# Optimization experiments

Hardware: AMD Instinct MI355X
Metric: run time of the kernel (lower is better)

## Reference

```python
import jax, jax.numpy as jnp
import numpy as np

N, M, D = 2048, 50000, 128


def setup_inputs() -> dict:
    key = jax.random.key(0)
    kz, kr = jax.random.split(key)
    z = jax.random.normal(kz, (N, D), dtype=jnp.float32)
    ref = jax.random.normal(kr, (M, D), dtype=jnp.float32)  # stands in for the concatenated in_dl batches
    return {"z": z, "ref": ref, "k": 10}


def reference(z, ref, k):
    # L2-normalize rows (matches z / z.norm(dim=1, keepdim=True))
    zn = z / jnp.linalg.norm(z, axis=1, keepdims=True)      # [N, D]
    rn = ref / jnp.linalg.norm(ref, axis=1, keepdims=True)  # [M, D]
    # Pairwise L2 distances via ||a||^2 + ||b||^2 - 2 a.b (same math as the
    # broadcast (rep_batch - rep_z).norm(dim=2), without the O(N*M*D) blowup).
    sq = (jnp.sum(zn * zn, axis=1)[:, None]
          + jnp.sum(rn * rn, axis=1)[None, :]
          - 2.0 * jnp.einsum('nd,md->nm', zn, rn))          # [N, M]
    dist = jnp.sqrt(jnp.maximum(sq, 1e-12))
    # Full sort along the reference axis, take the k-th smallest distance.
    return jnp.sort(dist, axis=1)[:, k]                      # [N]
```

## Files before the change

### kernel.cpp

```cpp
#include <hip/hip_runtime.h>


#define D_DIM 128
#define TQB 256
#define BR 64
#define NCH 64
#define NSUB (NCH * 32)
#define KK 11
#define NCAND 32
#define SLOTS 25
#define DNF 2816

typedef __bf16 bf16_t;
typedef bf16_t bf16x8 __attribute__((ext_vector_type(8)));
typedef float f32x16 __attribute__((ext_vector_type(16)));

__device__ __forceinline__ unsigned short f2bf(float f) {
    unsigned u = __float_as_uint(f);
    return (unsigned short)((u + 0x7fffu + ((u >> 16) & 1u)) >> 16);
}

__global__ __launch_bounds__(256) void normalize_bf16(
    const float* __restrict__ z, const float* __restrict__ ref,
    unsigned short* __restrict__ zb, unsigned short* __restrict__ rb,
    int N, int M)
{
    const int w = threadIdx.x >> 6;
    const int l = threadIdx.x & 63;
    const int row = blockIdx.x * 4 + w;
    if (row >= N + M) return;
    const float* in; unsigned short* out; int r;
    if (row < N) { in = z;   out = zb; r = row; }
    else         { in = ref; out = rb; r = row - N; }
    const float2 v = ((const float2*)in)[(size_t)r * 64 + l];
    float ss = v.x * v.x + v.y * v.y;
    #pragma unroll
    for (int off = 32; off > 0; off >>= 1) ss += __shfl_xor(ss, off);
    const float inv = rsqrtf(ss);
    ushort2 o; o.x = f2bf(v.x * inv); o.y = f2bf(v.y * inv);
    ((ushort2*)out)[(size_t)r * 64 + l] = o;
}

__device__ __forceinline__ void gld_lds16(const unsigned short* g,
                                          unsigned short* l) {
    __builtin_amdgcn_global_load_lds(
        (__attribute__((address_space(1))) void*)g,
        (__attribute__((address_space(3))) void*)l, 16, 0, 0);
}

__global__ __launch_bounds__(512) void knn_maxes(
    const unsigned short* __restrict__ zb, const unsigned short* __restrict__ rb,
    float* __restrict__ maxes, int N, int M, int chunk)
{
    __shared__ __align__(16) unsigned short Bt[2 * BR * D_DIM];

    const int nwg = 8 * NCH;
    const int bid = (int)blockIdx.x + 8 * (int)blockIdx.y;
    const int swz = (bid & 7) * (nwg >> 3) + (bid >> 3);
    const int bx = swz & 7;
    const int by = swz >> 3;

    const int t = threadIdx.x;
    const int lane = t & 63;
    const int w = t >> 6;
    const int quad = lane >> 4;
    const int ln = lane & 15;
    const int l31 = lane & 31;
    const int hi = lane >> 5;
    const int row = bx * TQB + w * 32 + l31;
    const int c0 = by * chunk;
    const int c1 = min(c0 + chunk, M);
    const int clen = c1 - c0;
    const int nt = (clen + BR - 1) / BR;

    bf16x8 qfr[8];
    #pragma unroll
    for (int ks = 0; ks < 8; ++ks)
        qfr[ks] = *(const bf16x8*)&zb[(size_t)row * D_DIM + ks * 16 + hi * 8];

    float mx[16];
    #pragma unroll
    for (int r = 0; r < 16; ++r) mx[r] = -3.0f;

    auto stage = [&](int half, int tile) {
        const int s0 = c0 + tile * BR;
        #pragma unroll
        for (int i = 0; i < 2; ++i) {
            const int r = w * 8 + i * 4 + quad;
            int g = s0 + r; if (g > M - 1) g = M - 1;
            const int sl = ln ^ (r & 15);
            gld_lds16(&rb[(size_t)g * D_DIM + sl * 8],
                      &Bt[half * (BR * D_DIM) + (w * 8 + i * 4) * D_DIM]);
        }
    };

    stage(0, 0);
    stage(1, nt > 1 ? 1 : 0);

    for (int it = 0; it < nt; ++it) {
        if (it + 1 < nt) asm volatile("s_waitcnt vmcnt(2)" ::: "memory");
        else             asm volatile("s_waitcnt vmcnt(0)" ::: "memory");
        __builtin_amdgcn_s_barrier();
        asm volatile("" ::: "memory");
        __builtin_amdgcn_sched_barrier(0);

        const int cur = it & 1;
        const unsigned short* Bc = &Bt[cur * (BR * D_DIM)];

        f32x16 acc0 = {0,0,0,0,0,0,0,0,0,0,0,0,0,0,0,0};
        f32x16 acc1 = {0,0,0,0,0,0,0,0,0,0,0,0,0,0,0,0};

        __builtin_amdgcn_s_setprio(1);
        #pragma unroll
        for (int ks = 0; ks < 8; ++ks) {
            const int sl = ((ks * 2 + hi) ^ ln) * 8;
            bf16x8 a0 = *(const bf16x8*)&Bc[(l31)      * D_DIM + sl];
            bf16x8 a1 = *(const bf16x8*)&Bc[(32 + l31) * D_DIM + sl];
            acc0 = __builtin_amdgcn_mfma_f32_32x32x16_bf16(a0, qfr[ks], acc0, 0, 0, 0);
            acc1 = __builtin_amdgcn_mfma_f32_32x32x16_bf16(a1, qfr[ks], acc1, 0, 0, 0);
        }
        __builtin_amdgcn_s_setprio(0);

        const int rem = clen - it * BR;
        if (rem >= BR) {
            #pragma unroll
            for (int r = 0; r < 16; ++r)
                mx[r] = fmaxf(mx[r], fmaxf(acc0[r], acc1[r]));
        } else {
            #pragma unroll
            for (int r = 0; r < 16; ++r) {
                const int crow = (r & 3) + 8 * (r >> 2) + 4 * hi;
                if (crow < rem)      mx[r] = fmaxf(mx[r], acc0[r]);
                if (32 + crow < rem) mx[r] = fmaxf(mx[r], acc1[r]);
            }
        }

        __builtin_amdgcn_sched_barrier(0);
        asm volatile("" ::: "memory");
        __builtin_amdgcn_s_barrier();
        if (it + 2 < nt) stage(cur, it + 2);
    }

    float* mp = &maxes[(size_t)row * NSUB + by * 32 + hi * 16];
    #pragma unroll
    for (int r4 = 0; r4 < 4; ++r4) {
        float4 v4 = { mx[r4 * 4], mx[r4 * 4 + 1], mx[r4 * 4 + 2], mx[r4 * 4 + 3] };
        *(float4*)&mp[r4 * 4] = v4;
    }
}

__device__ __forceinline__ float kth_largest_64(float* s, int kk, int lane) {
    float cur = -3.0f;
    for (int it = 0; it <= kk; ++it) {
        float m = s[0];
        #pragma unroll
        for (int off = 32; off > 0; off >>= 1) m = fmaxf(m, __shfl_xor(m, off));
        cur = m;
        unsigned long long b = __ballot(s[0] == m);
        bool owner = ((int)(__ffsll(b) - 1) == lane);
        #pragma unroll
        for (int j = 0; j < KK - 1; ++j) s[j] = owner ? s[j + 1] : s[j];
        if (owner) s[KK - 1] = -3.0f;
    }
    return cur;
}

__device__ __forceinline__ void wave_topk_to_lds(float* s, int kk, int lane,
                                                 float* dst) {
    for (int it = 0; it <= kk; ++it) {
        float m = s[0];
        #pragma unroll
        for (int off = 32; off > 0; off >>= 1) m = fmaxf(m, __shfl_xor(m, off));
        if (lane == 0) dst[it] = m;
        unsigned long long b = __ballot(s[0] == m);
        bool owner = ((int)(__ffsll(b) - 1) == lane);
        #pragma unroll
        for (int j = 0; j < KK - 1; ++j) s[j] = owner ? s[j + 1] : s[j];
        if (owner) s[KK - 1] = -3.0f;
    }
}

__global__ __launch_bounds__(256) void knn_select(
    const unsigned short* __restrict__ zb, const unsigned short* __restrict__ rb,
    const float* __restrict__ maxes, const int* __restrict__ kp,
    float* __restrict__ out, int M, int chunk)
{
    const int row = blockIdx.x;
    const int t = threadIdx.x;
    const int lane = t & 63;
    const int wv = t >> 6;
    __shared__ float dbuf[DNF];
    __shared__ float tops[4 * KK];
    __shared__ float T_s;
    __shared__ int cand_s[NCAND];
    __shared__ int cn_s;

    const int kk = *kp;
    if (t == 0) cn_s = 0;

    {
        float s[KK];
        #pragma unroll
        for (int j = 0; j < KK; ++j) s[j] = -3.0f;
        #pragma unroll
        for (int i = 0; i < NSUB / 256; ++i) {
            float v = maxes[(size_t)row * NSUB + wv * (NSUB / 4) + lane + 64 * i];
            #pragma unroll
            for (int j = 0; j < KK; ++j) {
                float hi = fmaxf(s[j], v), lo = fminf(s[j], v);
                s[j] = hi; v = lo;
            }
        }
        wave_topk_to_lds(s, kk, lane, &tops[wv * KK]);
    }

    const int gl = t & 7;
    const int grp = t >> 3;
    float q0r[8], q1r[8];
    {
        bf16x8 qv0 = *(const bf16x8*)&zb[(size_t)row * D_DIM + gl * 8];
        bf16x8 qv1 = *(const bf16x8*)&zb[(size_t)row * D_DIM + 64 + gl * 8];
        #pragma unroll
        for (int e = 0; e < 8; ++e) { q0r[e] = (float)qv0[e]; q1r[e] = (float)qv1[e]; }
    }
    __syncthreads();

    if (t < 64) {
        float s[KK];
        s[0] = (t < 4 * (kk + 1)) ? tops[t] : -3.0f;
        #pragma unroll
        for (int j = 1; j < KK; ++j) s[j] = -3.0f;
        const float T = kth_largest_64(s, kk, lane);
        if (t == 0) T_s = T;
    }
    __syncthreads();

    {
        const float T = T_s;
        #pragma unroll
        for (int i = 0; i < NSUB / 256; ++i) {
            int idx = wv * (NSUB / 4) + lane + 64 * i;
            float v = maxes[(size_t)row * NSUB + idx];
            if (v >= T) {
                int sl = atomicAdd(&cn_s, 1);
                if (sl < NCAND) cand_s[sl] = idx;
            }
        }
    }
    __syncthreads();

    const int cn = cn_s;
    const int slots = (chunk + 31) >> 5;
    int nsel;

    if (cn <= NCAND && slots <= SLOTS) {
        const int W = cn * slots;
        int ci = grp / slots;
        int sl = grp - ci * slots;
        for (int gs = grp; gs < W; gs += 32) {
            const int s  = cand_s[ci];
            const int by = s >> 5;
            const int h2 = (s >> 4) & 1;
            const int r  = s & 15;
            const int base = (r & 3) + 8 * (r >> 2) + 4 * h2;
            const int c0 = by * chunk;
            const int c1 = min(c0 + chunk, M);
            const int ref = c0 + sl * 32 + base;
            const bool valid = ref < c1;
            float p = 0.f;
            if (valid) {
                const unsigned short* rp = &rb[(size_t)ref * D_DIM + gl * 8];
                bf16x8 r0 = *(const bf16x8*)rp;
                bf16x8 r1 = *(const bf16x8*)(rp + 64);
                #pragma unroll
                for (int e = 0; e < 8; ++e) {
                    p = fmaf((float)r0[e], q0r[e], p);
                    p = fmaf((float)r1[e], q1r[e], p);
                }
            }
            p += __shfl_xor(p, 1);
            p += __shfl_xor(p, 2);
            p += __shfl_xor(p, 4);
            if (gl == 0) dbuf[gs] = valid ? p : -3.0f;
            sl += 32;
            while (sl >= slots) { sl -= slots; ++ci; }
        }
        nsel = W;
    } else {
        float s[KK];
        #pragma unroll
        for (int j = 0; j < KK; ++j) s[j] = -3.0f;
        for (int g = grp; g < M; g += 32) {
            const unsigned short* rp = &rb[(size_t)g * D_DIM + gl * 8];
            bf16x8 r0 = *(const bf16x8*)rp;
            bf16x8 r1 = *(const bf16x8*)(rp + 64);
            float p = 0.f;
            #pragma unroll
            for (int e = 0; e < 8; ++e) {
                p = fmaf((float)r0[e], q0r[e], p);
                p = fmaf((float)r1[e], q1r[e], p);
            }
            p += __shfl_xor(p, 1);
            p += __shfl_xor(p, 2);
            p += __shfl_xor(p, 4);
            #pragma unroll
            for (int j = 0; j < KK; ++j) {
                float hi = fmaxf(s[j], p), lo = fminf(s[j], p);
                s[j] = hi; p = lo;
            }
        }
        #pragma unroll
        for (int j = 0; j < KK; ++j) dbuf[t * KK + j] = s[j];
        nsel = DNF;
    }
    __syncthreads();

    if (t < 64) {
        float s[KK];
        #pragma unroll
        for (int j = 0; j < KK; ++j) s[j] = -3.0f;
        for (int j = t; j < nsel; j += 64) {
            float v = dbuf[j];
            #pragma unroll
            for (int q = 0; q < KK; ++q) {
                float hi = fmaxf(s[q], v), lo = fminf(s[q], v);
                s[q] = hi; v = lo;
            }
        }
        const float cur = kth_largest_64(s, kk, lane);
        if (t == 0) out[row] = sqrtf(fmaxf(2.0f - 2.0f * cur, 1e-12f));
    }
}

extern "C" void kernel_launch(void* const* d_in, const int* in_sizes, int n_in,
                              void* d_out, int out_size, void* d_ws, size_t ws_size,
                              hipStream_t stream) {
    const float* z   = (const float*)d_in[0];
    const float* ref = (const float*)d_in[1];
    const int*   kp  = (const int*)d_in[2];
    float* out = (float*)d_out;

    const int N = in_sizes[0] / D_DIM;
    const int M = in_sizes[1] / D_DIM;

    unsigned short* zbuf = (unsigned short*)d_ws;
    unsigned short* rbuf = zbuf + (size_t)N * D_DIM;
    float* maxes = (float*)(rbuf + (size_t)M * D_DIM);

    normalize_bf16<<<(N + M + 3) / 4, 256, 0, stream>>>(z, ref, zbuf, rbuf, N, M);

    const int chunk = (M + NCH - 1) / NCH;
    dim3 grid(N / TQB, NCH);

    knn_maxes<<<grid, 512, 0, stream>>>(zbuf, rbuf, maxes, N, M, chunk);
    knn_select<<<N, 256, 0, stream>>>(zbuf, rbuf, maxes, kp, out, M, chunk);
}
```

Measured before the change: 139.9 us.

## Track top-2 per subchunk to shrink candidate rescoring in selection

The first pass now keeps the largest and second-largest dot product per subchunk, not just the maximum, and writes both to a doubled maxes buffer. The selection kernel builds a threshold from the top-2 values and re-scores only subchunks whose second-largest value reaches that threshold. Since the top two of every other subchunk are already known exactly, far fewer reference rows should need bf16 dot products, and often none at all. In exchange, the main GEMM loop does extra max/min work per element, the intermediate buffer doubles in size, and there is an extra merge pass over the top-2 values.

```diff
diff --git a/kernel.cpp b/kernel.cpp
--- a/kernel.cpp
+++ b/kernel.cpp
@@ -7,7 +7,7 @@
 #define NCH 64
 #define NSUB (NCH * 32)
 #define KK 11
-#define NCAND 32
+#define NEXP 16
 #define SLOTS 25
 #define DNF 2816
 
@@ -48,6 +48,10 @@
         (__attribute__((address_space(3))) void*)l, 16, 0, 0);
 }
 
+#define TOP2(m1v, m2v, vv) do { float _v = (vv);                  \
+        (m2v) = fmaxf((m2v), fminf((m1v), _v));                   \
+        (m1v) = fmaxf((m1v), _v); } while (0)
+
 __global__ __launch_bounds__(512) void knn_maxes(
     const unsigned short* __restrict__ zb, const unsigned short* __restrict__ rb,
     float* __restrict__ maxes, int N, int M, int chunk)
@@ -78,9 +82,9 @@
     for (int ks = 0; ks < 8; ++ks)
         qfr[ks] = *(const bf16x8*)&zb[(size_t)row * D_DIM + ks * 16 + hi * 8];
 
-    float mx[16];
-    #pragma unroll
-    for (int r = 0; r < 16; ++r) mx[r] = -3.0f;
+    float m1[16], m2[16];
+    #pragma unroll
+    for (int r = 0; r < 16; ++r) { m1[r] = -3.0f; m2[r] = -3.0f; }
 
     auto stage = [&](int half, int tile) {
         const int s0 = c0 + tile * BR;
@@ -124,14 +128,16 @@
         const int rem = clen - it * BR;
         if (rem >= BR) {
             #pragma unroll
-            for (int r = 0; r < 16; ++r)
-                mx[r] = fmaxf(mx[r], fmaxf(acc0[r], acc1[r]));
+            for (int r = 0; r < 16; ++r) {
+                TOP2(m1[r], m2[r], acc0[r]);
+                TOP2(m1[r], m2[r], acc1[r]);
+            }
         } else {
             #pragma unroll
             for (int r = 0; r < 16; ++r) {
                 const int crow = (r & 3) + 8 * (r >> 2) + 4 * hi;
-                if (crow < rem)      mx[r] = fmaxf(mx[r], acc0[r]);
-                if (32 + crow < rem) mx[r] = fmaxf(mx[r], acc1[r]);
+                if (crow < rem)      { TOP2(m1[r], m2[r], acc0[r]); }
+                if (32 + crow < rem) { TOP2(m1[r], m2[r], acc1[r]); }
             }
         }
 
@@ -141,11 +147,14 @@
         if (it + 2 < nt) stage(cur, it + 2);
     }
 
-    float* mp = &maxes[(size_t)row * NSUB + by * 32 + hi * 16];
+    float* mp1 = &maxes[(size_t)row * NSUB + by * 32 + hi * 16];
+    float* mp2 = mp1 + (size_t)N * NSUB;
     #pragma unroll
     for (int r4 = 0; r4 < 4; ++r4) {
-        float4 v4 = { mx[r4 * 4], mx[r4 * 4 + 1], mx[r4 * 4 + 2], mx[r4 * 4 + 3] };
-        *(float4*)&mp[r4 * 4] = v4;
+        float4 v1 = { m1[r4*4], m1[r4*4+1], m1[r4*4+2], m1[r4*4+3] };
+        float4 v2 = { m2[r4*4], m2[r4*4+1], m2[r4*4+2], m2[r4*4+3] };
+        *(float4*)&mp1[r4 * 4] = v1;
+        *(float4*)&mp2[r4 * 4] = v2;
     }
 }
 
@@ -180,10 +189,18 @@
     }
 }
 
+__device__ __forceinline__ void sorted_insert(float* s, float v) {
+    #pragma unroll
+    for (int j = 0; j < KK; ++j) {
+        float hi = fmaxf(s[j], v), lo = fminf(s[j], v);
+        s[j] = hi; v = lo;
+    }
+}
+
 __global__ __launch_bounds__(256) void knn_select(
     const unsigned short* __restrict__ zb, const unsigned short* __restrict__ rb,
     const float* __restrict__ maxes, const int* __restrict__ kp,
-    float* __restrict__ out, int M, int chunk)
+    float* __restrict__ out, int N, int M, int chunk)
 {
     const int row = blockIdx.x;
     const int t = threadIdx.x;
@@ -192,11 +209,14 @@
     __shared__ float dbuf[DNF];
     __shared__ float tops[4 * KK];
     __shared__ float T_s;
-    __shared__ int cand_s[NCAND];
-    __shared__ int cn_s;
+    __shared__ int expl[NEXP];
+    __shared__ int ecnt;
 
     const int kk = *kp;
-    if (t == 0) cn_s = 0;
+    if (t == 0) ecnt = 0;
+
+    const float* m1p = maxes + (size_t)row * NSUB;
+    const float* m2p = m1p + (size_t)N * NSUB;
 
     {
         float s[KK];
@@ -204,14 +224,38 @@
         for (int j = 0; j < KK; ++j) s[j] = -3.0f;
         #pragma unroll
         for (int i = 0; i < NSUB / 256; ++i) {
-            float v = maxes[(size_t)row * NSUB + wv * (NSUB / 4) + lane + 64 * i];
-            #pragma unroll
-            for (int j = 0; j < KK; ++j) {
-                float hi = fmaxf(s[j], v), lo = fminf(s[j], v);
-                s[j] = hi; v = lo;
-            }
+            sorted_insert(s, m1p[wv * (NSUB / 4) + lane + 64 * i]);
+            sorted_insert(s, m2p[wv * (NSUB / 4) + lane + 64 * i]);
         }
         wave_topk_to_lds(s, kk, lane, &tops[wv * KK]);
+    }
+    __syncthreads();
+
+    if (t < 64) {
+        float s[KK];
+        s[0] = (t < 4 * (kk + 1)) ? tops[t] : -3.0f;
+        #pragma unroll
+        for (int j = 1; j < KK; ++j) s[j] = -3.0f;
+        const float T = kth_largest_64(s, kk, lane);
+        if (t == 0) T_s = T;
+    }
+    __syncthreads();
+    const float T0 = T_s;
+
+    #pragma unroll
+    for (int i = 0; i < NSUB / 256; ++i) {
+        int idx = wv * (NSUB / 4) + lane + 64 * i;
+        if (m2p[idx] >= T0) {
+            int e = atomicAdd(&ecnt, 1);
+            if (e < NEXP) expl[e] = idx;
+        }
+    }
+    __syncthreads();
+    const int en = ecnt;
+
+    if (en == 0) {
+        if (t == 0) out[row] = sqrtf(fmaxf(2.0f - 2.0f * T0, 1e-12f));
+        return;
     }
 
     const int gl = t & 7;
@@ -223,42 +267,16 @@
         #pragma unroll
         for (int e = 0; e < 8; ++e) { q0r[e] = (float)qv0[e]; q1r[e] = (float)qv1[e]; }
     }
-    __syncthreads();
-
-    if (t < 64) {
-        float s[KK];
-        s[0] = (t < 4 * (kk + 1)) ? tops[t] : -3.0f;
-        #pragma unroll
-        for (int j = 1; j < KK; ++j) s[j] = -3.0f;
-        const float T = kth_largest_64(s, kk, lane);
-        if (t == 0) T_s = T;
-    }
-    __syncthreads();
-
-    {
-        const float T = T_s;
-        #pragma unroll
-        for (int i = 0; i < NSUB / 256; ++i) {
-            int idx = wv * (NSUB / 4) + lane + 64 * i;
-            float v = maxes[(size_t)row * NSUB + idx];
-            if (v >= T) {
-                int sl = atomicAdd(&cn_s, 1);
-                if (sl < NCAND) cand_s[sl] = idx;
-            }
-        }
-    }
-    __syncthreads();
-
-    const int cn = cn_s;
+
     const int slots = (chunk + 31) >> 5;
     int nsel;
 
-    if (cn <= NCAND && slots <= SLOTS) {
-        const int W = cn * slots;
+    if (en <= NEXP && slots <= SLOTS) {
+        const int W = en * slots;
         int ci = grp / slots;
         int sl = grp - ci * slots;
         for (int gs = grp; gs < W; gs += 32) {
-            const int s  = cand_s[ci];
+            const int s  = expl[ci];
             const int by = s >> 5;
             const int h2 = (s >> 4) & 1;
             const int r  = s & 15;
@@ -285,8 +303,38 @@
             sl += 32;
             while (sl >= slots) { sl -= slots; ++ci; }
         }
+        __syncthreads();
+
+        {
+            float s[KK];
+            #pragma unroll
+            for (int j = 0; j < KK; ++j) s[j] = -3.0f;
+            #pragma unroll
+            for (int i = 0; i < NSUB / 256; ++i) {
+                int idx = wv * (NSUB / 4) + lane + 64 * i;
+                bool skip = false;
+                for (int j = 0; j < en && j < NEXP; ++j) skip |= (idx == expl[j]);
+                sorted_insert(s, skip ? -3.0f : m1p[idx]);
+                sorted_insert(s, skip ? -3.0f : m2p[idx]);
+            }
+            wave_topk_to_lds(s, kk, lane, &tops[wv * KK]);
+        }
         nsel = W;
-    } else {
+        __syncthreads();
+
+        if (t < 64) {
+            float s[KK];
+            s[0] = (t < 4 * (kk + 1)) ? tops[t] : -3.0f;
+            #pragma unroll
+            for (int j = 1; j < KK; ++j) s[j] = -3.0f;
+            for (int j = t; j < nsel; j += 64) sorted_insert(s, dbuf[j]);
+            const float cur = kth_largest_64(s, kk, lane);
+            if (t == 0) out[row] = sqrtf(fmaxf(2.0f - 2.0f * cur, 1e-12f));
+        }
+        return;
+    }
+
+    {
         float s[KK];
         #pragma unroll
         for (int j = 0; j < KK; ++j) s[j] = -3.0f;
@@ -303,30 +351,17 @@
             p += __shfl_xor(p, 1);
             p += __shfl_xor(p, 2);
             p += __shfl_xor(p, 4);
-            #pragma unroll
-            for (int j = 0; j < KK; ++j) {
-                float hi = fmaxf(s[j], p), lo = fminf(s[j], p);
-                s[j] = hi; p = lo;
-            }
+            sorted_insert(s, p);
         }
         #pragma unroll
         for (int j = 0; j < KK; ++j) dbuf[t * KK + j] = s[j];
-        nsel = DNF;
     }
     __syncthreads();
-
     if (t < 64) {
         float s[KK];
         #pragma unroll
         for (int j = 0; j < KK; ++j) s[j] = -3.0f;
-        for (int j = t; j < nsel; j += 64) {
-            float v = dbuf[j];
-            #pragma unroll
-            for (int q = 0; q < KK; ++q) {
-                float hi = fmaxf(s[q], v), lo = fminf(s[q], v);
-                s[q] = hi; v = lo;
-            }
-        }
+        for (int j = t; j < DNF; j += 64) sorted_insert(s, dbuf[j]);
         const float cur = kth_largest_64(s, kk, lane);
         if (t == 0) out[row] = sqrtf(fmaxf(2.0f - 2.0f * cur, 1e-12f));
     }
@@ -353,5 +388,5 @@
     dim3 grid(N / TQB, NCH);
 
     knn_maxes<<<grid, 512, 0, stream>>>(zbuf, rbuf, maxes, N, M, chunk);
-    knn_select<<<N, 256, 0, stream>>>(zbuf, rbuf, maxes, kp, out, M, chunk);
-}
+    knn_select<<<N, 256, 0, stream>>>(zbuf, rbuf, maxes, kp, out, N, M, chunk);
+}
```

Result: slower. 158.5 us (+13.3%).

## Track per-half-tile maxima in bf16 to tighten candidate buckets

Applied to the files above, without the earlier changes.

The maxes kernel now keeps separate running maxima for the two 32-row halves of each 64-row tile, doubling the number of buckets per query while storing them as bf16 so the buffer stays the same size. With finer buckets, each candidate covers fewer references (13 slots instead of 25), which cuts the exact rescoring work in the select kernel. The cost is extra registers and max operations in the GEMM loop, and bf16 rounding of the bucket maxima could in principle change which buckets pass the threshold. A sorted_insert helper replaces the repeated insertion loops.

```diff
diff --git a/kernel.cpp b/kernel.cpp
--- a/kernel.cpp
+++ b/kernel.cpp
@@ -5,10 +5,10 @@
 #define TQB 256
 #define BR 64
 #define NCH 64
-#define NSUB (NCH * 32)
+#define NSUB (NCH * 64)
 #define KK 11
 #define NCAND 32
-#define SLOTS 25
+#define SLOTS 13
 #define DNF 2816
 
 typedef __bf16 bf16_t;
@@ -18,6 +18,9 @@
 __device__ __forceinline__ unsigned short f2bf(float f) {
     unsigned u = __float_as_uint(f);
     return (unsigned short)((u + 0x7fffu + ((u >> 16) & 1u)) >> 16);
+}
+__device__ __forceinline__ float bf2f(unsigned short u) {
+    return __uint_as_float((unsigned)u << 16);
 }
 
 __global__ __launch_bounds__(256) void normalize_bf16(
@@ -50,7 +53,7 @@
 
 __global__ __launch_bounds__(512) void knn_maxes(
     const unsigned short* __restrict__ zb, const unsigned short* __restrict__ rb,
-    float* __restrict__ maxes, int N, int M, int chunk)
+    unsigned short* __restrict__ maxes, int N, int M, int chunk)
 {
     __shared__ __align__(16) unsigned short Bt[2 * BR * D_DIM];
 
@@ -78,9 +81,9 @@
     for (int ks = 0; ks < 8; ++ks)
         qfr[ks] = *(const bf16x8*)&zb[(size_t)row * D_DIM + ks * 16 + hi * 8];
 
-    float mx[16];
-    #pragma unroll
-    for (int r = 0; r < 16; ++r) mx[r] = -3.0f;
+    float mxA[16], mxB[16];
+    #pragma unroll
+    for (int r = 0; r < 16; ++r) { mxA[r] = -3.0f; mxB[r] = -3.0f; }
 
     auto stage = [&](int half, int tile) {
         const int s0 = c0 + tile * BR;
@@ -124,14 +127,16 @@
         const int rem = clen - it * BR;
         if (rem >= BR) {
             #pragma unroll
-            for (int r = 0; r < 16; ++r)
-                mx[r] = fmaxf(mx[r], fmaxf(acc0[r], acc1[r]));
+            for (int r = 0; r < 16; ++r) {
+                mxA[r] = fmaxf(mxA[r], acc0[r]);
+                mxB[r] = fmaxf(mxB[r], acc1[r]);
+            }
         } else {
             #pragma unroll
             for (int r = 0; r < 16; ++r) {
                 const int crow = (r & 3) + 8 * (r >> 2) + 4 * hi;
-                if (crow < rem)      mx[r] = fmaxf(mx[r], acc0[r]);
-                if (32 + crow < rem) mx[r] = fmaxf(mx[r], acc1[r]);
+                if (crow < rem)      mxA[r] = fmaxf(mxA[r], acc0[r]);
+                if (32 + crow < rem) mxB[r] = fmaxf(mxB[r], acc1[r]);
             }
         }
 
@@ -141,12 +146,14 @@
         if (it + 2 < nt) stage(cur, it + 2);
     }
 
-    float* mp = &maxes[(size_t)row * NSUB + by * 32 + hi * 16];
-    #pragma unroll
-    for (int r4 = 0; r4 < 4; ++r4) {
-        float4 v4 = { mx[r4 * 4], mx[r4 * 4 + 1], mx[r4 * 4 + 2], mx[r4 * 4 + 3] };
-        *(float4*)&mp[r4 * 4] = v4;
-    }
+    union { unsigned short u[16]; uint4 q[2]; } h0, h1;
+    #pragma unroll
+    for (int r = 0; r < 16; ++r) { h0.u[r] = f2bf(mxA[r]); h1.u[r] = f2bf(mxB[r]); }
+    unsigned short* mp = &maxes[(size_t)row * NSUB + by * 64 + hi * 16];
+    *(uint4*)&mp[0]      = h0.q[0];
+    *(uint4*)&mp[8]      = h0.q[1];
+    *(uint4*)&mp[32]     = h1.q[0];
+    *(uint4*)&mp[40]     = h1.q[1];
 }
 
 __device__ __forceinline__ float kth_largest_64(float* s, int kk, int lane) {
@@ -180,9 +187,17 @@
     }
 }
 
+__device__ __forceinline__ void sorted_insert(float* s, float v) {
+    #pragma unroll
+    for (int j = 0; j < KK; ++j) {
+        float hi = fmaxf(s[j], v), lo = fminf(s[j], v);
+        s[j] = hi; v = lo;
+    }
+}
+
 __global__ __launch_bounds__(256) void knn_select(
     const unsigned short* __restrict__ zb, const unsigned short* __restrict__ rb,
-    const float* __restrict__ maxes, const int* __restrict__ kp,
+    const unsigned short* __restrict__ maxes, const int* __restrict__ kp,
     float* __restrict__ out, int M, int chunk)
 {
     const int row = blockIdx.x;
@@ -198,19 +213,15 @@
     const int kk = *kp;
     if (t == 0) cn_s = 0;
 
+    const unsigned short* m1p = maxes + (size_t)row * NSUB;
+
     {
         float s[KK];
         #pragma unroll
         for (int j = 0; j < KK; ++j) s[j] = -3.0f;
         #pragma unroll
-        for (int i = 0; i < NSUB / 256; ++i) {
-            float v = maxes[(size_t)row * NSUB + wv * (NSUB / 4) + lane + 64 * i];
-            #pragma unroll
-            for (int j = 0; j < KK; ++j) {
-                float hi = fmaxf(s[j], v), lo = fminf(s[j], v);
-                s[j] = hi; v = lo;
-            }
-        }
+        for (int i = 0; i < NSUB / 256; ++i)
+            sorted_insert(s, bf2f(m1p[wv * (NSUB / 4) + lane + 64 * i]));
         wave_topk_to_lds(s, kk, lane, &tops[wv * KK]);
     }
 
@@ -240,8 +251,7 @@
         #pragma unroll
         for (int i = 0; i < NSUB / 256; ++i) {
             int idx = wv * (NSUB / 4) + lane + 64 * i;
-            float v = maxes[(size_t)row * NSUB + idx];
-            if (v >= T) {
+            if (bf2f(m1p[idx]) >= T) {
                 int sl = atomicAdd(&cn_s, 1);
                 if (sl < NCAND) cand_s[sl] = idx;
             }
@@ -250,7 +260,7 @@
     __syncthreads();
 
     const int cn = cn_s;
-    const int slots = (chunk + 31) >> 5;
+    const int slots = (chunk + BR - 1) / BR;
     int nsel;
 
     if (cn <= NCAND && slots <= SLOTS) {
@@ -258,14 +268,15 @@
         int ci = grp / slots;
         int sl = grp - ci * slots;
         for (int gs = grp; gs < W; gs += 32) {
-            const int s  = cand_s[ci];
-            const int by = s >> 5;
-            const int h2 = (s >> 4) & 1;
-            const int r  = s & 15;
-            const int base = (r & 3) + 8 * (r >> 2) + 4 * h2;
+            const int s    = cand_s[ci];
+            const int by   = s >> 6;
+            const int half = (s >> 5) & 1;
+            const int h2   = (s >> 4) & 1;
+            const int r    = s & 15;
+            const int off  = half * 32 + (r & 3) + 8 * (r >> 2) + 4 * h2;
             const int c0 = by * chunk;
             const int c1 = min(c0 + chunk, M);
-            const int ref = c0 + sl * 32 + base;
+            const int ref = c0 + sl * 64 + off;
             const bool valid = ref < c1;
             float p = 0.f;
             if (valid) {
@@ -303,11 +314,7 @@
             p += __shfl_xor(p, 1);
             p += __shfl_xor(p, 2);
             p += __shfl_xor(p, 4);
-            #pragma unroll
-            for (int j = 0; j < KK; ++j) {
-                float hi = fmaxf(s[j], p), lo = fminf(s[j], p);
-                s[j] = hi; p = lo;
-            }
+            sorted_insert(s, p);
         }
         #pragma unroll
         for (int j = 0; j < KK; ++j) dbuf[t * KK + j] = s[j];
@@ -319,14 +326,7 @@
         float s[KK];
         #pragma unroll
         for (int j = 0; j < KK; ++j) s[j] = -3.0f;
-        for (int j = t; j < nsel; j += 64) {
-            float v = dbuf[j];
-            #pragma unroll
-            for (int q = 0; q < KK; ++q) {
-                float hi = fmaxf(s[q], v), lo = fminf(s[q], v);
-                s[q] = hi; v = lo;
-            }
-        }
+        for (int j = t; j < nsel; j += 64) sorted_insert(s, dbuf[j]);
         const float cur = kth_largest_64(s, kk, lane);
         if (t == 0) out[row] = sqrtf(fmaxf(2.0f - 2.0f * cur, 1e-12f));
     }
@@ -345,7 +345,7 @@
 
     unsigned short* zbuf = (unsigned short*)d_ws;
     unsigned short* rbuf = zbuf + (size_t)N * D_DIM;
-    float* maxes = (float*)(rbuf + (size_t)M * D_DIM);
+    unsigned short* maxes = rbuf + (size_t)M * D_DIM;
 
     normalize_bf16<<<(N + M + 3) / 4, 256, 0, stream>>>(z, ref, zbuf, rbuf, N, M);
 
```

Result: slower. 147.9 us (+5.8%).
